# Kernel optimization log

Measured on AMD Instinct MI355X. Metric: run time of the kernel, lower is better.

Reference implementation:

```python
import jax, jax.numpy as jnp
import numpy as np
from jax import lax

KERNEL_EPS = 1e-4   # eps in softmax_kernel
ATTN_EPS = 1e-6     # eps in causal_linear_attention
CHUNK = 64          # chunk length for the causal scan


def softmax_kernel(data, projection_matrix, is_query):
    # data: [b,h,n,d], projection_matrix: [r,d]
    d = data.shape[-1]
    r = projection_matrix.shape[0]
    data_normalizer = d ** -0.25
    ratio = r ** -0.5
    data_dash = jnp.einsum('bhnd,rd->bhnr', data_normalizer * data, projection_matrix)
    diag_data = (jnp.sum(data ** 2, axis=-1) * 0.5 * data_normalizer ** 2)[..., None]  # [b,h,n,1]
    if is_query:
        stab = jnp.max(data_dash, axis=-1, keepdims=True)
    else:
        stab = jnp.max(data_dash)
    return ratio * (jnp.exp(data_dash - diag_data - stab) + KERNEL_EPS)


def causal_linear_attention(qp, kp, v, chunk=CHUNK, eps=ATTN_EPS):
    # qp,kp: [b,h,n,r] feature maps; v: [b,h,n,e]
    b, h, n, r = qp.shape
    e = v.shape[-1]
    nc = n // chunk
    # -> [nc, b, h, chunk, *] for lax.scan over chunks
    qs = jnp.moveaxis(qp.reshape(b, h, nc, chunk, r), 2, 0)
    ks = jnp.moveaxis(kp.reshape(b, h, nc, chunk, r), 2, 0)
    vs = jnp.moveaxis(v.reshape(b, h, nc, chunk, e), 2, 0)

    def step(carry, xs):
        k_last, ctx_last = carry  # [b,h,r], [b,h,r,e]
        qch, kch, vch = xs        # [b,h,c,r], [b,h,c,r], [b,h,c,e]
        k_cum = k_last[:, :, None, :] + jnp.cumsum(kch, axis=2)              # [b,h,c,r]
        D_inv = 1.0 / jnp.einsum('bhcr,bhcr->bhc', qch, k_cum + eps)         # [b,h,c]
        ctx = jnp.einsum('bhcr,bhce->bhcre', kch, vch)                       # [b,h,c,r,e]
        ctx_cum = ctx_last[:, :, None] + jnp.cumsum(ctx, axis=2)             # [b,h,c,r,e]
        out = jnp.einsum('bhcre,bhcr,bhc->bhce', ctx_cum, qch, D_inv)        # [b,h,c,e]
        return (k_cum[:, :, -1], ctx_cum[:, :, -1]), out

    init = (jnp.zeros((b, h, r), qp.dtype), jnp.zeros((b, h, r, e), qp.dtype))
    _, outs = lax.scan(step, init, (qs, ks, vs))  # outs: [nc,b,h,c,e]
    return jnp.moveaxis(outs, 0, 2).reshape(b, h, n, e)


def setup_inputs() -> dict:
    key = jax.random.key(0)
    kq, kk, kv, kp = jax.random.split(key, 4)
    b, h, n, d, r = 2, 8, 4096, 64, 256
    q = jax.random.normal(kq, (b, h, n, d), dtype=jnp.float32)
    k = jax.random.normal(kk, (b, h, n, d), dtype=jnp.float32)
    v = jax.random.normal(kv, (b, h, n, d), dtype=jnp.float32)
    projection_matrix = jax.random.normal(kp, (r, d), dtype=jnp.float32)
    return {"q": q, "k": k, "v": v, "projection_matrix": projection_matrix}


def reference(q, k, v, projection_matrix):
    qp = softmax_kernel(q, projection_matrix, is_query=True)
    kp = softmax_kernel(k, projection_matrix, is_query=False)
    return causal_linear_attention(qp, kp, v)
```

## Files before the change

kernel.cpp:

```cpp
#include <hip/hip_runtime.h>


typedef unsigned short ushort_t;
typedef __attribute__((ext_vector_type(8))) short bf16x8;
typedef __attribute__((ext_vector_type(4))) float f32x4;

#define KEPS 1e-4f
#define AEPS 1e-6f
#define NORMIZER 0.35355339059327373f
#define RATIO 0.0625f

__device__ __forceinline__ ushort_t bf16r(float f) {
  unsigned u = __float_as_uint(f);
  return (ushort_t)((u + 0x7fffu + ((u >> 16) & 1u)) >> 16);
}
__device__ __forceinline__ float ubf(ushort_t h) {
  return __uint_as_float((unsigned)h << 16);
}

__global__ __launch_bounds__(256) void pconv_kernel(
    const float* __restrict__ P, ushort_t* __restrict__ Phi,
    ushort_t* __restrict__ Plo)
{
  int idx = blockIdx.x * 1024 + threadIdx.x;
  #pragma unroll
  for (int p = 0; p < 4; ++p) {
    int i = idx + p * 256;
    float x = P[i];
    ushort_t h = bf16r(x);
    Phi[i] = h;
    Plo[i] = bf16r(x - ubf(h));
  }
}

__global__ __launch_bounds__(256, 4) void feat_mfma(
    const float* __restrict__ Q, const float* __restrict__ K,
    const ushort_t* __restrict__ Phi, const ushort_t* __restrict__ Plo,
    ushort_t* __restrict__ qp, ushort_t* __restrict__ E,
    float* __restrict__ bmax)
{
  __shared__ union {
    struct { ushort_t Xhi[64 * 72]; ushort_t Xlo[64 * 72]; } s;
    ushort_t outb[64 * 72];
  } u;
  __shared__ ushort_t Pq[2][64 * 72];
  __shared__ float diagS[64];
  __shared__ float redm[4];

  int bid = blockIdx.x, tid = threadIdx.x;
  bool isK = bid >= 1024;
  const float* X = isK ? K : Q;
  size_t rowbase = (size_t)(isK ? bid - 1024 : bid) * 64;

  #pragma unroll
  for (int p = 0; p < 4; ++p) {
    int idx = tid + p * 256;
    int row = idx >> 4, c4 = idx & 15;
    float4 x = *(const float4*)&X[(rowbase + row) * 64 + c4 * 4];
    ushort4 h, l;
    h.x = bf16r(x.x); l.x = bf16r(x.x - ubf(h.x));
    h.y = bf16r(x.y); l.y = bf16r(x.y - ubf(h.y));
    h.z = bf16r(x.z); l.z = bf16r(x.z - ubf(h.z));
    h.w = bf16r(x.w); l.w = bf16r(x.w - ubf(h.w));
    *(ushort4*)&u.s.Xhi[row * 72 + c4 * 4] = h;
    *(ushort4*)&u.s.Xlo[row * 72 + c4 * 4] = l;
    float ss = x.x * x.x + x.y * x.y + x.z * x.z + x.w * x.w;
    ss += __shfl_xor(ss, 1, 64); ss += __shfl_xor(ss, 2, 64);
    ss += __shfl_xor(ss, 4, 64); ss += __shfl_xor(ss, 8, 64);
    if ((tid & 15) == 0) diagS[row] = 0.0625f * ss;
  }
  __syncthreads();

  int lane = tid & 63, wv = tid >> 6;
  int n15 = lane & 15, quad = lane >> 4;

  bf16x8 ah[2], al[2];
  #pragma unroll
  for (int ks = 0; ks < 2; ++ks) {
    int off = (16 * wv + n15) * 72 + quad * 8 + 32 * ks;
    ah[ks] = *(const bf16x8*)&u.s.Xhi[off];
    al[ks] = *(const bf16x8*)&u.s.Xlo[off];
  }

  f32x4 acc[16];
  #pragma unroll
  for (int tc = 0; tc < 16; ++tc) acc[tc] = f32x4{0.f, 0.f, 0.f, 0.f};

  #pragma unroll
  for (int q4 = 0; q4 < 4; ++q4) {
    if (q4) __syncthreads();
    #pragma unroll
    for (int t = 0; t < 2; ++t) {
      int f = tid + t * 256;
      int cl = f >> 3, k8 = (f & 7) * 8;
      size_t g = (size_t)(q4 * 64 + cl) * 64 + k8;
      *(bf16x8*)&Pq[0][cl * 72 + k8] = *(const bf16x8*)&Phi[g];
      *(bf16x8*)&Pq[1][cl * 72 + k8] = *(const bf16x8*)&Plo[g];
    }
    __syncthreads();
    #pragma unroll
    for (int tcl = 0; tcl < 4; ++tcl) {
      f32x4 a = acc[q4 * 4 + tcl];
      #pragma unroll
      for (int ks = 0; ks < 2; ++ks) {
        int off = (16 * tcl + n15) * 72 + quad * 8 + 32 * ks;
        bf16x8 bh = *(const bf16x8*)&Pq[0][off];
        bf16x8 bl = *(const bf16x8*)&Pq[1][off];
        a = __builtin_amdgcn_mfma_f32_16x16x32_bf16(ah[ks], bh, a, 0, 0, 0);
        a = __builtin_amdgcn_mfma_f32_16x16x32_bf16(ah[ks], bl, a, 0, 0, 0);
        a = __builtin_amdgcn_mfma_f32_16x16x32_bf16(al[ks], bh, a, 0, 0, 0);
      }
      acc[q4 * 4 + tcl] = a;
    }
  }

  float dg[4];
  #pragma unroll
  for (int r = 0; r < 4; ++r) dg[r] = diagS[16 * wv + quad * 4 + r];

  float sub[4];
  if (!isK) {
    #pragma unroll
    for (int r = 0; r < 4; ++r) {
      float mx = -3.0e38f;
      #pragma unroll
      for (int tc = 0; tc < 16; ++tc) mx = fmaxf(mx, acc[tc][r]);
      #pragma unroll
      for (int s = 1; s < 16; s <<= 1) mx = fmaxf(mx, __shfl_xor(mx, s, 64));
      sub[r] = dg[r] + NORMIZER * mx;
    }
  } else {
    float bm = -3.0e38f;
    #pragma unroll
    for (int tc = 0; tc < 16; ++tc)
      #pragma unroll
      for (int r = 0; r < 4; ++r) bm = fmaxf(bm, acc[tc][r]);
    #pragma unroll
    for (int s = 1; s < 64; s <<= 1) bm = fmaxf(bm, __shfl_xor(bm, s, 64));
    if (lane == 0) redm[wv] = bm;
    #pragma unroll
    for (int r = 0; r < 4; ++r) sub[r] = dg[r];
  }

  ushort_t* dst = (isK ? E : qp) + rowbase * 256;
  #pragma unroll
  for (int qt = 0; qt < 4; ++qt) {
    __syncthreads();
    #pragma unroll
    for (int t4 = 0; t4 < 4; ++t4) {
      int tc = qt * 4 + t4;
      #pragma unroll
      for (int r = 0; r < 4; ++r) {
        int row = 16 * wv + quad * 4 + r;
        float ex = __expf(NORMIZER * acc[tc][r] - sub[r]);
        float val = isK ? ex : RATIO * (ex + KEPS);
        u.outb[row * 72 + t4 * 16 + n15] = bf16r(val);
      }
    }
    __syncthreads();
    int row = tid >> 2, c0 = (tid & 3) * 16;
    bf16x8 v0 = *(const bf16x8*)&u.outb[row * 72 + c0];
    bf16x8 v1 = *(const bf16x8*)&u.outb[row * 72 + c0 + 8];
    *(bf16x8*)&dst[row * 256 + qt * 64 + c0] = v0;
    *(bf16x8*)&dst[row * 256 + qt * 64 + c0 + 8] = v1;
  }

  if (isK && tid == 0) {
    float m4 = fmaxf(fmaxf(redm[0], redm[1]), fmaxf(redm[2], redm[3]));
    bmax[bid - 1024] = NORMIZER * m4;
  }
}

__global__ __launch_bounds__(256) void kmax_reduce(
    const float* __restrict__ bmax, float* __restrict__ kmax)
{
  __shared__ float red[4];
  int tid = threadIdx.x;
  float m = fmaxf(fmaxf(bmax[tid], bmax[tid + 256]),
                  fmaxf(bmax[tid + 512], bmax[tid + 768]));
  #pragma unroll
  for (int s = 1; s < 64; s <<= 1) m = fmaxf(m, __shfl_xor(m, s, 64));
  if ((tid & 63) == 0) red[tid >> 6] = m;
  __syncthreads();
  if (tid == 0)
    *kmax = fmaxf(fmaxf(red[0], red[1]), fmaxf(red[2], red[3]));
}

__global__ __launch_bounds__(256) void chunksum_mfma(
    const ushort_t* __restrict__ E, const float* __restrict__ V,
    ushort_t* __restrict__ SE, float* __restrict__ zE, float* __restrict__ SV)
{
  __shared__ ushort_t Et[256 * 72];
  __shared__ ushort_t Vt[64 * 72];
  __shared__ float red2[256];

  int bc = blockIdx.x, tid = threadIdx.x;
  size_t ebase = (size_t)bc * 16384;

  #pragma unroll
  for (int p = 0; p < 8; ++p) {
    int g = (tid + p * 256) * 8;
    int pos = g >> 8, j0 = g & 255;
    bf16x8 ev = *(const bf16x8*)&E[ebase + g];
    #pragma unroll
    for (int jj = 0; jj < 8; ++jj) {
      int j = j0 + jj;
      int pr = (pos + 8 * ((j >> 3) & 7)) & 63;
      Et[j * 72 + pr] = (ushort_t)ev[jj];
    }
  }
  float vsum = 0.f;
  #pragma unroll
  for (int p = 0; p < 16; ++p) {
    int g = tid + p * 256;
    int pos = g >> 6, e = g & 63;
    float x = V[(size_t)bc * 4096 + g];
    vsum += x;
    int pr = (pos + 8 * ((e >> 3) & 7)) & 63;
    Vt[e * 72 + pr] = bf16r(x);
  }
  red2[tid] = vsum;
  __syncthreads();
  if (tid < 64)
    SV[(size_t)bc * 64 + tid] =
        red2[tid] + red2[64 + tid] + red2[128 + tid] + red2[192 + tid];

  {
    float s = 0.f;
    #pragma unroll
    for (int m8 = 0; m8 < 8; ++m8) {
      bf16x8 r8 = *(const bf16x8*)&Et[tid * 72 + m8 * 8];
      #pragma unroll
      for (int x = 0; x < 8; ++x) s += ubf((ushort_t)r8[x]);
    }
    zE[(size_t)bc * 256 + tid] = s;
  }

  int lane = tid & 63, wv = tid >> 6;
  int n15 = lane & 15, quad = lane >> 4;

  bf16x8 aV[2];
  {
    int e = 16 * wv + n15;
    int rot = 8 * ((e >> 3) & 7);
    #pragma unroll
    for (int ks = 0; ks < 2; ++ks) {
      int pr = (quad * 8 + 32 * ks + rot) & 63;
      aV[ks] = *(const bf16x8*)&Vt[e * 72 + pr];
    }
  }

  f32x4 acc[16];
  #pragma unroll
  for (int tc = 0; tc < 16; ++tc) {
    int j = 16 * tc + n15;
    int rot = 8 * ((j >> 3) & 7);
    f32x4 a = {0.f, 0.f, 0.f, 0.f};
    #pragma unroll
    for (int ks = 0; ks < 2; ++ks) {
      int pr = (quad * 8 + 32 * ks + rot) & 63;
      bf16x8 b = *(const bf16x8*)&Et[j * 72 + pr];
      a = __builtin_amdgcn_mfma_f32_16x16x32_bf16(aV[ks], b, a, 0, 0, 0);
    }
    acc[tc] = a;
  }
  __syncthreads();

  ushort_t* outS = Et;
  #pragma unroll
  for (int tc = 0; tc < 16; ++tc)
    #pragma unroll
    for (int r = 0; r < 4; ++r) {
      int e = 16 * wv + quad * 4 + r;
      outS[e * 264 + 16 * tc + n15] = bf16r(acc[tc][r]);
    }
  __syncthreads();
  #pragma unroll
  for (int p = 0; p < 8; ++p) {
    int g = (tid + p * 256) * 8;
    int e = g >> 8, j0 = g & 255;
    bf16x8 vv = *(const bf16x8*)&outS[e * 264 + j0];
    *(bf16x8*)&SE[ebase + g] = vv;
  }
}

__global__ __launch_bounds__(256) void prefix_kernel(
    ushort_t* __restrict__ S, float* __restrict__ zE,
    const float* __restrict__ SV, const float* __restrict__ kmax)
{
  int b = blockIdx.x;
  float m = *kmax;
  float c1 = RATIO * __expf(-m);
  const float c0 = RATIO * KEPS;
  if (b < 1024) {
    int flat = b * 256 + threadIdx.x;
    int bh = flat >> 14;
    int idx = flat & 16383;
    int e = idx >> 8;
    size_t base = (size_t)bh * 1048576 + idx;
    const float* svp = SV + (size_t)bh * 4096 + e;
    float runE = 0.f, runV = 0.f;
    for (int cc = 0; cc < 64; cc += 8) {
      ushort_t t[8]; float sv[8];
      #pragma unroll
      for (int u2 = 0; u2 < 8; ++u2) {
        t[u2] = S[base + (size_t)(cc + u2) * 16384];
        sv[u2] = svp[(size_t)(cc + u2) * 64];
      }
      #pragma unroll
      for (int u2 = 0; u2 < 8; ++u2) {
        S[base + (size_t)(cc + u2) * 16384] = bf16r(c1 * runE + c0 * runV);
        runE += ubf(t[u2]);
        runV += sv[u2];
      }
    }
  } else {
    int bh = b - 1024;
    int j = threadIdx.x;
    size_t base = (size_t)bh * 16384 + j;
    float run = 0.f;
    for (int cc = 0; cc < 64; cc += 8) {
      float t[8];
      #pragma unroll
      for (int u2 = 0; u2 < 8; ++u2)
        t[u2] = zE[base + (size_t)(cc + u2) * 256];
      #pragma unroll
      for (int u2 = 0; u2 < 8; ++u2) {
        zE[base + (size_t)(cc + u2) * 256] = run;
        run += c1 * t[u2] + 64.0f * c0;
      }
    }
  }
}

__device__ __forceinline__ void stage_tile(const ushort_t* __restrict__ gt,
                                           ushort_t* lds0, int tid, int wv) {
  #pragma unroll
  for (int i = 0; i < 2; ++i) {
    int D = i * 256 + tid;
    int row = D >> 5, cl = D & 31;
    int sc = (row << 5) | (cl ^ (row & 7));
    __builtin_amdgcn_global_load_lds(
        (const __attribute__((address_space(1))) void*)(gt + sc * 8),
        (__attribute__((address_space(3))) void*)(lds0 + (i * 256 + wv * 64) * 8),
        16, 0, 0);
  }
}

__global__ __launch_bounds__(256) void fused_mfma(
    const ushort_t* __restrict__ qp, const ushort_t* __restrict__ E,
    const float* __restrict__ kmax, const float* __restrict__ Z,
    const ushort_t* __restrict__ S, const float* __restrict__ V,
    float* __restrict__ out)
{
  __shared__ ushort_t As[64 * 72];
  __shared__ ushort_t Vt[64 * 72];
  __shared__ ushort_t Bst[2][4096];
  __shared__ float zv[256];
  __shared__ float qsumS[64];
  __shared__ float dqS[64];

  int bc = blockIdx.x, tid = threadIdx.x;
  int lane = tid & 63, wv = tid >> 6;
  int n15 = lane & 15, quad = lane >> 4;
  float m = *kmax;
  float c1 = RATIO * __expf(-m);
  const float c0 = RATIO * KEPS;
  size_t base = (size_t)bc * 16384;

  zv[tid] = Z[(size_t)bc * 256 + tid] + AEPS;
  #pragma unroll
  for (int p = 0; p < 16; ++p) {
    int idx = tid + p * 256;
    int t = idx >> 6, e = idx & 63;
    Vt[e * 72 + t] = bf16r(V[(size_t)bc * 4096 + idx]);
  }
  __syncthreads();

  stage_tile(E + base, &Bst[0][0], tid, wv);

  bf16x8 aQ[8];
  #pragma unroll
  for (int ks = 0; ks < 8; ++ks)
    aQ[ks] = *(const bf16x8*)&qp[base + (size_t)(16 * wv + n15) * 256 + quad * 8 + 32 * ks];

  float qsum = 0.f, dq = 0.f;
  #pragma unroll
  for (int ks = 0; ks < 8; ++ks)
    #pragma unroll
    for (int j = 0; j < 8; ++j) {
      float qv = ubf((ushort_t)aQ[ks][j]);
      qsum += qv;
      dq += qv * zv[quad * 8 + 32 * ks + j];
    }
  qsum += __shfl_xor(qsum, 16, 64); qsum += __shfl_xor(qsum, 32, 64);
  dq   += __shfl_xor(dq, 16, 64);   dq   += __shfl_xor(dq, 32, 64);
  if (quad == 0) { qsumS[16 * wv + n15] = qsum; dqS[16 * wv + n15] = dq; }

  float rs[4] = {0.f, 0.f, 0.f, 0.f};
  float dinv[4] = {0.f, 0.f, 0.f, 0.f};

  #pragma unroll
  for (int t = 0; t < 8; ++t) {
    asm volatile("s_waitcnt vmcnt(0)" ::: "memory");
    __builtin_amdgcn_s_barrier();
    if (t < 7) {
      const ushort_t* gt = (t < 3) ? (E + base + (size_t)(t + 1) * 4096)
                                   : (S + base + (size_t)(t - 3) * 4096);
      stage_tile(gt, &Bst[(t + 1) & 1][0], tid, wv);
    }

    bf16x8 bf[8];
    #pragma unroll
    for (int ks = 0; ks < 8; ++ks) {
      int rc = (4 * ks + quad) ^ (n15 & 7);
      bf[ks] = *(const bf16x8*)&Bst[t & 1][(n15 * 32 + rc) * 8];
    }
    f32x4 g = {0.f, 0.f, 0.f, 0.f};
    #pragma unroll
    for (int ks = 0; ks < 8; ++ks)
      g = __builtin_amdgcn_mfma_f32_16x16x32_bf16(aQ[ks], bf[ks], g, 0, 0, 0);

    if (t < 4) {
      int tc = t;
      #pragma unroll
      for (int r = 0; r < 4; ++r) {
        int i = 16 * wv + quad * 4 + r;
        int tt = 16 * tc + n15;
        float val = (tt <= i) ? (c1 * g[r] + c0 * qsumS[i]) : 0.f;
        As[i * 72 + tt] = bf16r(val);
        rs[r] += val;
      }
      if (t == 3) {
        #pragma unroll
        for (int r = 0; r < 4; ++r) {
          float v2 = rs[r];
          #pragma unroll
          for (int s = 1; s < 16; s <<= 1) v2 += __shfl_xor(v2, s, 64);
          int i = 16 * wv + quad * 4 + r;
          dinv[r] = 1.f / (dqS[i] + v2);
        }
      }
    } else {
      int ec = t - 4;
      f32x4 o = g;
      #pragma unroll
      for (int ks = 0; ks < 2; ++ks) {
        bf16x8 a2 = *(const bf16x8*)&As[(16 * wv + n15) * 72 + quad * 8 + 32 * ks];
        bf16x8 b2 = *(const bf16x8*)&Vt[(16 * ec + n15) * 72 + quad * 8 + 32 * ks];
        o = __builtin_amdgcn_mfma_f32_16x16x32_bf16(a2, b2, o, 0, 0, 0);
      }
      #pragma unroll
      for (int r = 0; r < 4; ++r) {
        int i = 16 * wv + quad * 4 + r;
        out[(size_t)bc * 4096 + (size_t)i * 64 + 16 * ec + n15] = o[r] * dinv[r];
      }
    }
  }
}

extern "C" void kernel_launch(void* const* d_in, const int* in_sizes, int n_in,
                              void* d_out, int out_size, void* d_ws, size_t ws_size,
                              hipStream_t stream)
{
  const float* q = (const float*)d_in[0];
  const float* k = (const float*)d_in[1];
  const float* v = (const float*)d_in[2];
  const float* P = (const float*)d_in[3];
  float* out = (float*)d_out;

  ushort_t* qp  = (ushort_t*)d_ws;
  ushort_t* E   = qp + 16777216;
  ushort_t* S   = E + 16777216;
  float*    zE  = (float*)(S + 16777216);
  float*    SV  = zE + 262144;
  ushort_t* Phi = (ushort_t*)(SV + 65536);
  ushort_t* Plo = Phi + 16384;
  float*    bmax = (float*)(Plo + 16384);
  float*    kmax = bmax + 1024;

  pconv_kernel<<<16, 256, 0, stream>>>(P, Phi, Plo);
  feat_mfma<<<2048, 256, 0, stream>>>(q, k, Phi, Plo, qp, E, bmax);
  kmax_reduce<<<1, 256, 0, stream>>>(bmax, kmax);
  chunksum_mfma<<<1024, 256, 0, stream>>>(E, v, S, zE, SV);
  prefix_kernel<<<1040, 256, 0, stream>>>(S, zE, SV, kmax);
  fused_mfma<<<1024, 256, 0, stream>>>(qp, E, kmax, zE, S, v, out);
}
```

Before: 168.8 us.

## Double-buffer projection tiles via async global-to-LDS loads and widen output staging

Projection hi/lo tiles in the feature kernel are now streamed into two XOR-swizzled LDS buffers with global_load_lds, prefetching the next tile while MFMAs run on the current one. This replaces the synchronous register-staged loads and the barrier between each chunk. The hi and lo passes are split into separate tiles and the MFMA order changes slightly. The output is written through one full-width LDS buffer with a single barrier instead of four rounds. LDS usage per block rises, which may limit occupancy.

```diff
diff --git a/kernel.cpp b/kernel.cpp
--- a/kernel.cpp
+++ b/kernel.cpp
@@ -33,6 +33,21 @@
   }
 }
 
+__device__ __forceinline__ void stage_ptile(const ushort_t* __restrict__ gt,
+                                            ushort_t* lds0, int tid) {
+  int wv = tid >> 6, lane = tid & 63;
+  #pragma unroll
+  for (int i = 0; i < 2; ++i) {
+    int D = i * 256 + wv * 64 + lane;
+    int row = D >> 3, c3 = D & 7;
+    int sc = (row << 3) | (c3 ^ (row & 7));
+    __builtin_amdgcn_global_load_lds(
+        (const __attribute__((address_space(1))) void*)(gt + sc * 8),
+        (__attribute__((address_space(3))) void*)(lds0 + (i * 256 + wv * 64) * 8),
+        16, 0, 0);
+  }
+}
+
 __global__ __launch_bounds__(256, 4) void feat_mfma(
     const float* __restrict__ Q, const float* __restrict__ K,
     const ushort_t* __restrict__ Phi, const ushort_t* __restrict__ Plo,
@@ -40,10 +55,13 @@
     float* __restrict__ bmax)
 {
   __shared__ union {
-    struct { ushort_t Xhi[64 * 72]; ushort_t Xlo[64 * 72]; } s;
-    ushort_t outb[64 * 72];
+    struct {
+      ushort_t Xhi[64 * 72];
+      ushort_t Xlo[64 * 72];
+      ushort_t Pt[2][4096];
+    } s;
+    ushort_t outb[64 * 268];
   } u;
-  __shared__ ushort_t Pq[2][64 * 72];
   __shared__ float diagS[64];
   __shared__ float redm[4];
 
@@ -51,6 +69,8 @@
   bool isK = bid >= 1024;
   const float* X = isK ? K : Q;
   size_t rowbase = (size_t)(isK ? bid - 1024 : bid) * 64;
+
+  stage_ptile(Phi, &u.s.Pt[0][0], tid);
 
   #pragma unroll
   for (int p = 0; p < 4; ++p) {
@@ -86,32 +106,35 @@
   #pragma unroll
   for (int tc = 0; tc < 16; ++tc) acc[tc] = f32x4{0.f, 0.f, 0.f, 0.f};
 
-  #pragma unroll
-  for (int q4 = 0; q4 < 4; ++q4) {
-    if (q4) __syncthreads();
-    #pragma unroll
-    for (int t = 0; t < 2; ++t) {
-      int f = tid + t * 256;
-      int cl = f >> 3, k8 = (f & 7) * 8;
-      size_t g = (size_t)(q4 * 64 + cl) * 64 + k8;
-      *(bf16x8*)&Pq[0][cl * 72 + k8] = *(const bf16x8*)&Phi[g];
-      *(bf16x8*)&Pq[1][cl * 72 + k8] = *(const bf16x8*)&Plo[g];
-    }
-    __syncthreads();
+  int buf = 0;
+  #pragma unroll
+  for (int t = 0; t < 8; ++t) {
+    int q4 = t >> 1;
+    bool isLo = t & 1;
+    if (t) {
+      asm volatile("s_waitcnt vmcnt(0)" ::: "memory");
+      __builtin_amdgcn_s_barrier();
+    }
+    if (t < 7) {
+      int tn = t + 1;
+      const ushort_t* gt = ((tn & 1) ? Plo : Phi) + (size_t)(tn >> 1) * 4096;
+      stage_ptile(gt, &u.s.Pt[buf ^ 1][0], tid);
+    }
     #pragma unroll
     for (int tcl = 0; tcl < 4; ++tcl) {
       f32x4 a = acc[q4 * 4 + tcl];
       #pragma unroll
       for (int ks = 0; ks < 2; ++ks) {
-        int off = (16 * tcl + n15) * 72 + quad * 8 + 32 * ks;
-        bf16x8 bh = *(const bf16x8*)&Pq[0][off];
-        bf16x8 bl = *(const bf16x8*)&Pq[1][off];
-        a = __builtin_amdgcn_mfma_f32_16x16x32_bf16(ah[ks], bh, a, 0, 0, 0);
-        a = __builtin_amdgcn_mfma_f32_16x16x32_bf16(ah[ks], bl, a, 0, 0, 0);
-        a = __builtin_amdgcn_mfma_f32_16x16x32_bf16(al[ks], bh, a, 0, 0, 0);
+        int jr = 16 * tcl + n15;
+        int rc = (quad + 4 * ks) ^ (n15 & 7);
+        bf16x8 b = *(const bf16x8*)&u.s.Pt[buf][jr * 64 + rc * 8];
+        a = __builtin_amdgcn_mfma_f32_16x16x32_bf16(ah[ks], b, a, 0, 0, 0);
+        if (!isLo)
+          a = __builtin_amdgcn_mfma_f32_16x16x32_bf16(al[ks], b, a, 0, 0, 0);
       }
       acc[q4 * 4 + tcl] = a;
     }
+    buf ^= 1;
   }
 
   float dg[4];
@@ -142,27 +165,25 @@
     for (int r = 0; r < 4; ++r) sub[r] = dg[r];
   }
 
+  __syncthreads();
   ushort_t* dst = (isK ? E : qp) + rowbase * 256;
   #pragma unroll
-  for (int qt = 0; qt < 4; ++qt) {
-    __syncthreads();
-    #pragma unroll
-    for (int t4 = 0; t4 < 4; ++t4) {
-      int tc = qt * 4 + t4;
-      #pragma unroll
-      for (int r = 0; r < 4; ++r) {
-        int row = 16 * wv + quad * 4 + r;
-        float ex = __expf(NORMIZER * acc[tc][r] - sub[r]);
-        float val = isK ? ex : RATIO * (ex + KEPS);
-        u.outb[row * 72 + t4 * 16 + n15] = bf16r(val);
-      }
-    }
-    __syncthreads();
-    int row = tid >> 2, c0 = (tid & 3) * 16;
-    bf16x8 v0 = *(const bf16x8*)&u.outb[row * 72 + c0];
-    bf16x8 v1 = *(const bf16x8*)&u.outb[row * 72 + c0 + 8];
-    *(bf16x8*)&dst[row * 256 + qt * 64 + c0] = v0;
-    *(bf16x8*)&dst[row * 256 + qt * 64 + c0 + 8] = v1;
+  for (int tc = 0; tc < 16; ++tc) {
+    #pragma unroll
+    for (int r = 0; r < 4; ++r) {
+      int row = 16 * wv + quad * 4 + r;
+      float ex = __expf(NORMIZER * acc[tc][r] - sub[r]);
+      float val = isK ? ex : RATIO * (ex + KEPS);
+      u.outb[row * 268 + 16 * tc + n15] = bf16r(val);
+    }
+  }
+  __syncthreads();
+  #pragma unroll
+  for (int p = 0; p < 8; ++p) {
+    int g = (tid + p * 256) * 8;
+    int row = g >> 8, c0 = g & 255;
+    bf16x8 v0 = *(const bf16x8*)&u.outb[row * 268 + c0];
+    *(bf16x8*)&dst[row * 256 + c0] = v0;
   }
 
   if (isK && tid == 0) {
```

New measurement: 166.8 us. Within noise of the previous version (-1.2%).
